# Kernel tuning notes

Hardware: AMD Instinct MI355X
Metric: run time of the kernel (lower is better)

## Reference

```python
import math
import jax, jax.numpy as jnp
import numpy as np

SHAPES = [(80, 80), (40, 40), (20, 20), (10, 10)]
BS, LQ, D, NH, NL, NP = 8, 1000, 256, 8, 4, 4
C = D // NH


def _offset_bias():
    # replicates _reset_parameters grid_init bias for sampling_offsets
    thetas = np.arange(NH, dtype=np.float32) * (2.0 * math.pi / NH)
    grid = np.stack([np.cos(thetas), np.sin(thetas)], -1)  # [NH,2]
    grid = grid / np.abs(grid).max(-1, keepdims=True)
    grid = np.tile(grid[:, None, None, :], (1, NL, NP, 1))  # [NH,NL,NP,2]
    for i in range(NP):
        grid[:, :, i, :] *= i + 1
    return jnp.asarray(grid.reshape(-1))


def setup_inputs() -> dict:
    key = jax.random.key(0)
    ks = jax.random.split(key, 8)
    len_v = sum(h * w for h, w in SHAPES)
    s = 1.0 / math.sqrt(D)
    starts = np.cumsum([0] + [h * w for h, w in SHAPES])[:-1]
    return {
        "query": jax.random.normal(ks[0], (BS, LQ, D), jnp.float32),
        "reference_points": jax.random.uniform(ks[1], (BS, LQ, NL, 2), jnp.float32),
        "value": jax.random.normal(ks[2], (BS, len_v, D), jnp.float32),
        "w_off": jax.random.normal(ks[3], (D, NH * NL * NP * 2), jnp.float32) * 0.01,
        "b_off": _offset_bias(),
        "w_attn": jax.random.normal(ks[4], (D, NH * NL * NP), jnp.float32) * 0.01,
        "b_attn": jnp.zeros((NH * NL * NP,), jnp.float32),
        "w_v": jax.random.normal(ks[5], (D, D), jnp.float32) * s,
        "b_v": jnp.zeros((D,), jnp.float32),
        "w_o": jax.random.normal(ks[6], (D, D), jnp.float32) * s,
        "b_o": jnp.zeros((D,), jnp.float32),
        "value_spatial_shapes": jnp.array(SHAPES, jnp.int32),
        "value_level_start_index": jnp.array(starts, jnp.int32),
    }


def _sample(img, grid, H, W):
    # bilinear grid_sample, padding_mode='zeros', align_corners=False
    # img: [B, C, H*W], grid: [B, Q, P, 2] in [-1, 1] -> out [B, C, Q, P]
    x = (grid[..., 0] + 1.0) * (W * 0.5) - 0.5
    y = (grid[..., 1] + 1.0) * (H * 0.5) - 0.5
    x0 = jnp.floor(x)
    y0 = jnp.floor(y)
    fx = x - x0
    fy = y - y0
    x0i = x0.astype(jnp.int32)
    y0i = y0.astype(jnp.int32)

    def gather(xi, yi, w):
        valid = (xi >= 0) & (xi < W) & (yi >= 0) & (yi < H)
        idx = jnp.clip(yi, 0, H - 1) * W + jnp.clip(xi, 0, W - 1)
        B, Q, P = idx.shape
        g = jax.vmap(lambda im, ix: im[:, ix])(img, idx.reshape(B, Q * P))  # [B,C,QP]
        return g.reshape(B, -1, Q, P) * (w * valid)[:, None]

    return (gather(x0i, y0i, (1 - fx) * (1 - fy))
            + gather(x0i + 1, y0i, fx * (1 - fy))
            + gather(x0i, y0i + 1, (1 - fx) * fy)
            + gather(x0i + 1, y0i + 1, fx * fy))


def _forward(query, reference_points, value, w_off, b_off, w_attn, b_attn,
             w_v, b_v, w_o, b_o, shapes):
    bs, lq, _ = query.shape
    v = (value @ w_v + b_v).reshape(bs, -1, NH, C)  # [bs, len_v, NH, C]
    off = (query @ w_off + b_off).reshape(bs, lq, NH, NL, NP, 2)
    attn = jax.nn.softmax((query @ w_attn + b_attn).reshape(bs, lq, NH, NL * NP), axis=-1)
    attn = attn.reshape(bs, lq, NH, NL, NP)
    # offset normalizer is spatial_shapes flipped -> (W, H) per level
    norm = jnp.array([[w, h] for h, w in shapes], dtype=query.dtype)  # [NL,2]
    loc = reference_points[:, :, None, :, None, :] + off / norm[None, None, None, :, None, :]
    grids = 2.0 * loc - 1.0  # [bs,lq,NH,NL,NP,2]
    start = 0
    sampled = []
    for lvl, (H, W) in enumerate(shapes):
        v_l = v[:, start:start + H * W].transpose(0, 2, 3, 1).reshape(bs * NH, C, H * W)
        g_l = grids[:, :, :, lvl].transpose(0, 2, 1, 3, 4).reshape(bs * NH, lq, NP, 2)
        sampled.append(_sample(v_l, g_l, H, W))  # [bs*NH, C, lq, NP]
        start += H * W
    samp = jnp.stack(sampled, axis=3).reshape(bs * NH, C, lq, NL * NP)
    aw = attn.transpose(0, 2, 1, 3, 4).reshape(bs * NH, 1, lq, NL * NP)
    out = (samp * aw).sum(-1).reshape(bs, NH * C, lq).transpose(0, 2, 1)  # [bs,lq,D]
    return out @ w_o + b_o


def reference(query, reference_points, value, w_off, b_off, w_attn, b_attn,
              w_v, b_v, w_o, b_o, value_spatial_shapes, value_level_start_index):
    shapes = [tuple(int(x) for x in r) for r in np.asarray(value_spatial_shapes)]
    return _forward(query, reference_points, value, w_off, b_off, w_attn, b_attn,
                    w_v, b_v, w_o, b_o, shapes)
```

## Files before the change

kernel.cpp:

```cpp
#include <hip/hip_runtime.h>
#include <hip/hip_bf16.h>
#include <math.h>

#define BS     8
#define LQ     1000
#define DMODEL 256
#define NH     8
#define NLV    4
#define NPT    4
#define LEN_V  8500
#define NQ     (BS*LQ)
#define MV     (BS*LEN_V)
#define KS     8

typedef __attribute__((ext_vector_type(8))) short short8;
typedef __attribute__((ext_vector_type(4))) float floatx4;

static __device__ __forceinline__ unsigned short f2bf(float f) {
    __hip_bfloat16 h = __float2bfloat16(f);
    return __builtin_bit_cast(unsigned short, h);
}
static __device__ __forceinline__ float asf(unsigned int u) {
    return __builtin_bit_cast(float, u);
}

static __device__ __forceinline__ void dma16(const unsigned short* g, unsigned short* lds) {
    __builtin_amdgcn_global_load_lds(
        (const __attribute__((address_space(1))) unsigned int*)g,
        (__attribute__((address_space(3))) unsigned int*)lds,
        16, 0, 0);
}

template <bool A32>
static __device__ __forceinline__ void gemm_core(
    const void* __restrict__ Aptr, const unsigned short* __restrict__ Bfrag,
    const float* __restrict__ bias1, const float* __restrict__ bias2, int nsplit,
    void* __restrict__ Cptr, int M, int N, int bn, int bm_start, int bm_stride,
    bool outbf, unsigned short (*As)[16384])
{
    const int tid = threadIdx.x;
    const int l   = tid & 63;
    const int w   = tid >> 6;
    const int lm  = l & 15;
    const int lk  = l >> 4;
    const int x7  = lm & 7;
    const int n_mtiles = (M + 63) >> 6;

    short8 Bf[2][KS];
    const int u0 = bn * 8 + w * 2;
    #pragma unroll
    for (int j = 0; j < 2; ++j)
        #pragma unroll
        for (int s = 0; s < KS; ++s)
            Bf[j][s] = *(const short8*)(Bfrag + ((size_t)((u0 + j) * KS + s) * 64 + l) * 8);

    auto aoff = [&](int tile, int j) -> size_t {
        const int slot = j * 256 + tid;
        const int row  = slot >> 5;
        const int gc   = (slot & 31) ^ (row & 7);
        int grow = tile * 64 + row; grow = grow < M ? grow : M - 1;
        return (size_t)grow * 256 + gc * 8;
    };

    float4 ra[8][2];

    int bm  = bm_start;
    int buf = 0;
    if (bm < n_mtiles) {
        if constexpr (A32) {
            #pragma unroll
            for (int j = 0; j < 8; ++j) {
                const float* s = (const float*)Aptr + aoff(bm, j);
                ra[j][0] = *(const float4*)s;
                ra[j][1] = *(const float4*)(s + 4);
            }
        } else {
            #pragma unroll
            for (int j = 0; j < 8; ++j)
                dma16((const unsigned short*)Aptr + aoff(bm, j),
                      &As[0][(j * 256 + w * 64) * 8]);
        }
    }

    while (bm < n_mtiles) {
        const int bm_next = bm + bm_stride;

        if constexpr (A32) {
            #pragma unroll
            for (int j = 0; j < 8; ++j) {
                const int slot = j * 256 + tid;
                short8 o;
                o[0] = (short)f2bf(ra[j][0].x); o[1] = (short)f2bf(ra[j][0].y);
                o[2] = (short)f2bf(ra[j][0].z); o[3] = (short)f2bf(ra[j][0].w);
                o[4] = (short)f2bf(ra[j][1].x); o[5] = (short)f2bf(ra[j][1].y);
                o[6] = (short)f2bf(ra[j][1].z); o[7] = (short)f2bf(ra[j][1].w);
                *(short8*)&As[buf][slot * 8] = o;
            }
            if (bm_next < n_mtiles) {
                #pragma unroll
                for (int j = 0; j < 8; ++j) {
                    const float* s = (const float*)Aptr + aoff(bm_next, j);
                    ra[j][0] = *(const float4*)s;
                    ra[j][1] = *(const float4*)(s + 4);
                }
            }
            __syncthreads();
        } else {
            __builtin_amdgcn_s_waitcnt(0);
            __syncthreads();
            if (bm_next < n_mtiles) {
                #pragma unroll
                for (int j = 0; j < 8; ++j)
                    dma16((const unsigned short*)Aptr + aoff(bm_next, j),
                          &As[buf ^ 1][(j * 256 + w * 64) * 8]);
            }
        }

        floatx4 acc[4][2];
        #pragma unroll
        for (int i = 0; i < 4; ++i)
            #pragma unroll
            for (int j = 0; j < 2; ++j)
                #pragma unroll
                for (int r = 0; r < 4; ++r) acc[i][j][r] = 0.f;

        #pragma unroll
        for (int s = 0; s < KS; ++s) {
            short8 afr[4];
            #pragma unroll
            for (int i = 0; i < 4; ++i)
                afr[i] = *(const short8*)(
                    &As[buf][(i * 16 + lm) * 256 + (((s * 4 + lk) ^ x7)) * 8]);
            #pragma unroll
            for (int i = 0; i < 4; ++i)
                #pragma unroll
                for (int j = 0; j < 2; ++j)
                    acc[i][j] = __builtin_amdgcn_mfma_f32_16x16x32_bf16(
                                    afr[i], Bf[j][s], acc[i][j], 0, 0, 0);
        }

        #pragma unroll
        for (int j = 0; j < 2; ++j) {
            const int col = bn * 128 + w * 32 + j * 16 + lm;
            const float bv = (bias2 != nullptr && col >= nsplit) ? bias2[col - nsplit]
                                                                 : bias1[col];
            #pragma unroll
            for (int i = 0; i < 4; ++i) {
                const int rbase = bm * 64 + i * 16 + lk * 4;
                #pragma unroll
                for (int r = 0; r < 4; ++r) {
                    const int row = rbase + r;
                    if (row < M) {
                        const float v = acc[i][j][r] + bv;
                        if (outbf)
                            ((unsigned short*)Cptr)[(size_t)row * N + col] = f2bf(v);
                        else
                            ((float*)Cptr)[(size_t)row * N + col] = v;
                    }
                }
            }
        }

        buf ^= 1;
        bm = bm_next;
    }
}

__global__ __launch_bounds__(256, 2) void gemm_fused(
    const float* __restrict__ value, const float* __restrict__ query,
    const unsigned short* __restrict__ wv_f, const unsigned short* __restrict__ woa_f,
    const float* __restrict__ b_v, const float* __restrict__ b_off,
    const float* __restrict__ b_attn,
    unsigned short* __restrict__ v_proj, float* __restrict__ offattn)
{
    __shared__ unsigned short As[2][16384];
    int bx = blockIdx.x;
    if (bx < 1064) {
        const int bm0 = bx % 532, bn = bx / 532;
        gemm_core<true>(value, wv_f, b_v, nullptr, 1 << 30,
                        v_proj, MV, 256, bn, bm0, 532, true, As);
    } else {
        bx -= 1064;
        const int bm0 = bx % 125, bn = bx / 125;
        gemm_core<true>(query, woa_f, b_off, b_attn, 256,
                        offattn, NQ, 384, bn, bm0, 125, false, As);
    }
}

__global__ __launch_bounds__(256, 2) void gemm_out(
    const unsigned short* __restrict__ out_pre, const unsigned short* __restrict__ wo_f,
    const float* __restrict__ b_o, float* __restrict__ out)
{
    __shared__ unsigned short As[2][16384];
    gemm_core<false>(out_pre, wo_f, b_o, nullptr, 1 << 30,
                     out, NQ, 256, blockIdx.y, blockIdx.x, 125, false, As);
}

__global__ __launch_bounds__(256) void prep_w(
    const float* __restrict__ w_v, const float* __restrict__ w_off,
    const float* __restrict__ w_attn, const float* __restrict__ w_o,
    unsigned short* __restrict__ wv_f, unsigned short* __restrict__ woa_f,
    unsigned short* __restrict__ wo_f)
{
    const int gid = blockIdx.x * 256 + threadIdx.x;
    int chunk, mode;
    if (gid < 8192)               { chunk = gid;         mode = 0; }
    else if (gid < 8192 + 12288)  { chunk = gid - 8192;  mode = 1; }
    else                          { chunk = gid - 20480; mode = 2; }
    const int l = chunk & 63, s = (chunk >> 6) & 7, u = chunk >> 9;
    short8 o;
    #pragma unroll
    for (int j = 0; j < 8; ++j) {
        const int k = s * 32 + (l >> 4) * 8 + j;
        const int n = u * 16 + (l & 15);
        float v;
        if (mode == 0)      v = w_v[k * 256 + n];
        else if (mode == 1) v = (n < 256) ? w_off[k * 256 + n] : w_attn[k * 128 + (n - 256)];
        else                v = w_o[k * 256 + n];
        o[j] = (short)f2bf(v);
    }
    unsigned short* dp = (mode == 0 ? wv_f : mode == 1 ? woa_f : wo_f)
                         + ((size_t)(u * 8 + s) * 64 + l) * 8;
    *(short8*)dp = o;
}

__global__ __launch_bounds__(512) void ms_sample_split(
    const unsigned short* __restrict__ v,
    const float* __restrict__ offattn,
    const float* __restrict__ refp,
    unsigned short* __restrict__ out_pre)
{
    __shared__ float offx_s[8][16][8];
    __shared__ float offy_s[8][16][8];
    __shared__ float atw_s [8][16][8];
    __shared__ float ref_s [8][8];
    __shared__ float part  [8][32][9];

    const int tid  = threadIdx.x;
    const int bswz = blockIdx.x & 7;
    const int iq0  = bswz * 1000 + (blockIdx.x >> 3) * 8;

    if (tid < 64) {
        const int q = tid >> 3, h = tid & 7;
        const float* rowp = offattn + (size_t)(iq0 + q) * 384;
        float lg[16];
        float m = -1e30f;
        #pragma unroll
        for (int i = 0; i < 16; ++i) { lg[i] = rowp[256 + h * 16 + i]; m = fmaxf(m, lg[i]); }
        float s = 0.f;
        #pragma unroll
        for (int i = 0; i < 16; ++i) { lg[i] = __expf(lg[i] - m); s += lg[i]; }
        const float inv = 1.f / s;
        #pragma unroll
        for (int i = 0; i < 16; ++i) atw_s[q][i][h] = lg[i] * inv;
        #pragma unroll
        for (int i = 0; i < 16; ++i) {
            offx_s[q][i][h] = rowp[(h * 16 + i) * 2 + 0];
            offy_s[q][i][h] = rowp[(h * 16 + i) * 2 + 1];
        }
        if (h == 0) {
            #pragma unroll
            for (int i = 0; i < 8; ++i) ref_s[q][i] = refp[(size_t)(iq0 + q) * 8 + i];
        }
    }
    __syncthreads();

    const int q8   = tid >> 6;
    const int half = (tid >> 5) & 1;
    const int sub  = tid & 31;
    const int h    = sub >> 2;
    const int oct  = sub & 3;

    float acc[8] = {0.f, 0.f, 0.f, 0.f, 0.f, 0.f, 0.f, 0.f};
    const unsigned short* vb = v + (size_t)bswz * LEN_V * 256 + h * 32 + oct * 8;
    const int Hs[4] = {80, 40, 20, 10};
    const int st[4] = {0, 6400, 8000, 8400};

    #pragma unroll
    for (int li = 0; li < 2; ++li) {
        const int lvl = half * 2 + li;
        const int W = Hs[lvl];
        const float bx = ref_s[q8][lvl * 2 + 0] * (float)W - 0.5f;
        const float by = ref_s[q8][lvl * 2 + 1] * (float)W - 0.5f;
        const unsigned short* vl = vb + (size_t)st[lvl] * 256;
        #pragma unroll
        for (int p = 0; p < NPT; ++p) {
            const int lp = lvl * 4 + p;
            const float x  = bx + offx_s[q8][lp][h];
            const float y  = by + offy_s[q8][lp][h];
            const float at = atw_s[q8][lp][h];
            const float x0f = floorf(x), y0f = floorf(y);
            const float fx = x - x0f, fy = y - y0f;
            const int x0 = (int)x0f, y0 = (int)y0f;
            const int x1 = x0 + 1,   y1 = y0 + 1;
            const int cx0 = min(max(x0, 0), W - 1);
            const int cx1 = min(max(x1, 0), W - 1);
            const int cy0 = min(max(y0, 0), W - 1);
            const int cy1 = min(max(y1, 0), W - 1);
            const float vx0 = (x0 >= 0 && x0 < W) ? 1.f : 0.f;
            const float vx1 = (x1 >= 0 && x1 < W) ? 1.f : 0.f;
            const float vy0 = (y0 >= 0 && y0 < W) ? 1.f : 0.f;
            const float vy1 = (y1 >= 0 && y1 < W) ? 1.f : 0.f;
            const float w00 = at * (1.f - fx) * (1.f - fy) * vx0 * vy0;
            const float w01 = at * fx * (1.f - fy) * vx1 * vy0;
            const float w10 = at * (1.f - fx) * fy * vx0 * vy1;
            const float w11 = at * fx * fy * vx1 * vy1;
            const unsigned short* r0 = vl + (size_t)(cy0 * W) * 256;
            const unsigned short* r1 = vl + (size_t)(cy1 * W) * 256;
            const uint4 d00 = *(const uint4*)(r0 + (size_t)cx0 * 256);
            const uint4 d01 = *(const uint4*)(r0 + (size_t)cx1 * 256);
            const uint4 d10 = *(const uint4*)(r1 + (size_t)cx0 * 256);
            const uint4 d11 = *(const uint4*)(r1 + (size_t)cx1 * 256);
            acc[0] += w00 * asf(d00.x << 16) + w01 * asf(d01.x << 16)
                    + w10 * asf(d10.x << 16) + w11 * asf(d11.x << 16);
            acc[1] += w00 * asf(d00.x & 0xffff0000u) + w01 * asf(d01.x & 0xffff0000u)
                    + w10 * asf(d10.x & 0xffff0000u) + w11 * asf(d11.x & 0xffff0000u);
            acc[2] += w00 * asf(d00.y << 16) + w01 * asf(d01.y << 16)
                    + w10 * asf(d10.y << 16) + w11 * asf(d11.y << 16);
            acc[3] += w00 * asf(d00.y & 0xffff0000u) + w01 * asf(d01.y & 0xffff0000u)
                    + w10 * asf(d10.y & 0xffff0000u) + w11 * asf(d11.y & 0xffff0000u);
            acc[4] += w00 * asf(d00.z << 16) + w01 * asf(d01.z << 16)
                    + w10 * asf(d10.z << 16) + w11 * asf(d11.z << 16);
            acc[5] += w00 * asf(d00.z & 0xffff0000u) + w01 * asf(d01.z & 0xffff0000u)
                    + w10 * asf(d10.z & 0xffff0000u) + w11 * asf(d11.z & 0xffff0000u);
            acc[6] += w00 * asf(d00.w << 16) + w01 * asf(d01.w << 16)
                    + w10 * asf(d10.w << 16) + w11 * asf(d11.w << 16);
            acc[7] += w00 * asf(d00.w & 0xffff0000u) + w01 * asf(d01.w & 0xffff0000u)
                    + w10 * asf(d10.w & 0xffff0000u) + w11 * asf(d11.w & 0xffff0000u);
        }
    }

    if (half == 1) {
        #pragma unroll
        for (int j = 0; j < 8; ++j) part[q8][sub][j] = acc[j];
    }
    __syncthreads();
    if (half == 0) {
        short8 o;
        #pragma unroll
        for (int j = 0; j < 8; ++j) o[j] = (short)f2bf(acc[j] + part[q8][sub][j]);
        *(short8*)(out_pre + (size_t)(iq0 + q8) * 256 + sub * 8) = o;
    }
}

extern "C" void kernel_launch(void* const* d_in, const int* in_sizes, int n_in,
                              void* d_out, int out_size, void* d_ws, size_t ws_size,
                              hipStream_t stream)
{
    const float* query  = (const float*)d_in[0];
    const float* refp   = (const float*)d_in[1];
    const float* value  = (const float*)d_in[2];
    const float* w_off  = (const float*)d_in[3];
    const float* b_off  = (const float*)d_in[4];
    const float* w_attn = (const float*)d_in[5];
    const float* b_attn = (const float*)d_in[6];
    const float* w_v    = (const float*)d_in[7];
    const float* b_v    = (const float*)d_in[8];
    const float* w_o    = (const float*)d_in[9];
    const float* b_o    = (const float*)d_in[10];
    (void)d_in[11]; (void)d_in[12];

    float* out = (float*)d_out;

    char* ws = (char*)d_ws;
    unsigned short* v_proj  = (unsigned short*)ws;
    float*          offattn = (float*)(ws + 34816000);
    unsigned short* out_pre = (unsigned short*)(ws + 47104000);
    unsigned short* wv_f    = (unsigned short*)(ws + 51200000);
    unsigned short* woa_f   = (unsigned short*)(ws + 51331072);
    unsigned short* wo_f    = (unsigned short*)(ws + 51527680);

    dim3 blk(256);

    hipLaunchKernelGGL(prep_w, dim3(112), blk, 0, stream,
                       w_v, w_off, w_attn, w_o, wv_f, woa_f, wo_f);
    hipLaunchKernelGGL(gemm_fused, dim3(1439), blk, 0, stream,
                       value, query, wv_f, woa_f, b_v, b_off, b_attn, v_proj, offattn);
    hipLaunchKernelGGL(ms_sample_split, dim3(1000), dim3(512), 0, stream,
                       v_proj, offattn, refp, out_pre);
    hipLaunchKernelGGL(gemm_out, dim3(125, 2), blk, 0, stream,
                       out_pre, wo_f, b_o, out);
}
```

Baseline: 197.1 us.

## Replace persistent double-buffered GEMM loop with one-tile-per-block GEMM kernels

```diff
diff --git a/kernel.cpp b/kernel.cpp
--- a/kernel.cpp
+++ b/kernel.cpp
@@ -32,11 +32,11 @@
 }
 
 template <bool A32>
-static __device__ __forceinline__ void gemm_core(
+static __device__ __forceinline__ void gemm_tile(
     const void* __restrict__ Aptr, const unsigned short* __restrict__ Bfrag,
     const float* __restrict__ bias1, const float* __restrict__ bias2, int nsplit,
-    void* __restrict__ Cptr, int M, int N, int bn, int bm_start, int bm_stride,
-    bool outbf, unsigned short (*As)[16384])
+    void* __restrict__ Cptr, int M, int N, int bn, int bm,
+    bool outbf, unsigned short* As )
 {
     const int tid = threadIdx.x;
     const int l   = tid & 63;
@@ -44,156 +44,125 @@
     const int lm  = l & 15;
     const int lk  = l >> 4;
     const int x7  = lm & 7;
-    const int n_mtiles = (M + 63) >> 6;
-
-    short8 Bf[2][KS];
-    const int u0 = bn * 8 + w * 2;
-    #pragma unroll
-    for (int j = 0; j < 2; ++j)
-        #pragma unroll
-        for (int s = 0; s < KS; ++s)
-            Bf[j][s] = *(const short8*)(Bfrag + ((size_t)((u0 + j) * KS + s) * 64 + l) * 8);
-
-    auto aoff = [&](int tile, int j) -> size_t {
+
+    auto aoff = [&](int j) -> size_t {
         const int slot = j * 256 + tid;
         const int row  = slot >> 5;
         const int gc   = (slot & 31) ^ (row & 7);
-        int grow = tile * 64 + row; grow = grow < M ? grow : M - 1;
+        int grow = bm * 64 + row; grow = grow < M ? grow : M - 1;
         return (size_t)grow * 256 + gc * 8;
     };
 
     float4 ra[8][2];
-
-    int bm  = bm_start;
-    int buf = 0;
-    if (bm < n_mtiles) {
-        if constexpr (A32) {
+    if constexpr (A32) {
+        #pragma unroll
+        for (int j = 0; j < 8; ++j) {
+            const float* s = (const float*)Aptr + aoff(j);
+            ra[j][0] = *(const float4*)s;
+            ra[j][1] = *(const float4*)(s + 4);
+        }
+    } else {
+        #pragma unroll
+        for (int j = 0; j < 8; ++j)
+            dma16((const unsigned short*)Aptr + aoff(j),
+                  &As[(j * 256 + w * 64) * 8]);
+    }
+
+    short8 Bf[2][KS];
+    const int u0 = bn * 8 + w * 2;
+    #pragma unroll
+    for (int j = 0; j < 2; ++j)
+        #pragma unroll
+        for (int s = 0; s < KS; ++s)
+            Bf[j][s] = *(const short8*)(Bfrag + ((size_t)((u0 + j) * KS + s) * 64 + l) * 8);
+
+    if constexpr (A32) {
+        #pragma unroll
+        for (int j = 0; j < 8; ++j) {
+            short8 o;
+            o[0] = (short)f2bf(ra[j][0].x); o[1] = (short)f2bf(ra[j][0].y);
+            o[2] = (short)f2bf(ra[j][0].z); o[3] = (short)f2bf(ra[j][0].w);
+            o[4] = (short)f2bf(ra[j][1].x); o[5] = (short)f2bf(ra[j][1].y);
+            o[6] = (short)f2bf(ra[j][1].z); o[7] = (short)f2bf(ra[j][1].w);
+            *(short8*)&As[(j * 256 + tid) * 8] = o;
+        }
+    } else {
+        __builtin_amdgcn_s_waitcnt(0);
+    }
+    __syncthreads();
+
+    floatx4 acc[4][2];
+    #pragma unroll
+    for (int i = 0; i < 4; ++i)
+        #pragma unroll
+        for (int j = 0; j < 2; ++j)
             #pragma unroll
-            for (int j = 0; j < 8; ++j) {
-                const float* s = (const float*)Aptr + aoff(bm, j);
-                ra[j][0] = *(const float4*)s;
-                ra[j][1] = *(const float4*)(s + 4);
-            }
-        } else {
-            #pragma unroll
-            for (int j = 0; j < 8; ++j)
-                dma16((const unsigned short*)Aptr + aoff(bm, j),
-                      &As[0][(j * 256 + w * 64) * 8]);
-        }
-    }
-
-    while (bm < n_mtiles) {
-        const int bm_next = bm + bm_stride;
-
-        if constexpr (A32) {
-            #pragma unroll
-            for (int j = 0; j < 8; ++j) {
-                const int slot = j * 256 + tid;
-                short8 o;
-                o[0] = (short)f2bf(ra[j][0].x); o[1] = (short)f2bf(ra[j][0].y);
-                o[2] = (short)f2bf(ra[j][0].z); o[3] = (short)f2bf(ra[j][0].w);
-                o[4] = (short)f2bf(ra[j][1].x); o[5] = (short)f2bf(ra[j][1].y);
-                o[6] = (short)f2bf(ra[j][1].z); o[7] = (short)f2bf(ra[j][1].w);
-                *(short8*)&As[buf][slot * 8] = o;
-            }
-            if (bm_next < n_mtiles) {
-                #pragma unroll
-                for (int j = 0; j < 8; ++j) {
-                    const float* s = (const float*)Aptr + aoff(bm_next, j);
-                    ra[j][0] = *(const float4*)s;
-                    ra[j][1] = *(const float4*)(s + 4);
-                }
-            }
-            __syncthreads();
-        } else {
-            __builtin_amdgcn_s_waitcnt(0);
-            __syncthreads();
-            if (bm_next < n_mtiles) {
-                #pragma unroll
-                for (int j = 0; j < 8; ++j)
-                    dma16((const unsigned short*)Aptr + aoff(bm_next, j),
-                          &As[buf ^ 1][(j * 256 + w * 64) * 8]);
-            }
-        }
-
-        floatx4 acc[4][2];
+            for (int r = 0; r < 4; ++r) acc[i][j][r] = 0.f;
+
+    #pragma unroll
+    for (int s = 0; s < KS; ++s) {
+        short8 afr[4];
+        #pragma unroll
+        for (int i = 0; i < 4; ++i)
+            afr[i] = *(const short8*)(
+                &As[(i * 16 + lm) * 256 + (((s * 4 + lk) ^ x7)) * 8]);
         #pragma unroll
         for (int i = 0; i < 4; ++i)
             #pragma unroll
             for (int j = 0; j < 2; ++j)
-                #pragma unroll
-                for (int r = 0; r < 4; ++r) acc[i][j][r] = 0.f;
-
-        #pragma unroll
-        for (int s = 0; s < KS; ++s) {
-            short8 afr[4];
+                acc[i][j] = __builtin_amdgcn_mfma_f32_16x16x32_bf16(
+                                afr[i], Bf[j][s], acc[i][j], 0, 0, 0);
+    }
+
+    #pragma unroll
+    for (int j = 0; j < 2; ++j) {
+        const int col = bn * 128 + w * 32 + j * 16 + lm;
+        const float bv = (bias2 != nullptr && col >= nsplit) ? bias2[col - nsplit]
+                                                             : bias1[col];
+        #pragma unroll
+        for (int i = 0; i < 4; ++i) {
+            const int rbase = bm * 64 + i * 16 + lk * 4;
             #pragma unroll
-            for (int i = 0; i < 4; ++i)
-                afr[i] = *(const short8*)(
-                    &As[buf][(i * 16 + lm) * 256 + (((s * 4 + lk) ^ x7)) * 8]);
-            #pragma unroll
-            for (int i = 0; i < 4; ++i)
-                #pragma unroll
-                for (int j = 0; j < 2; ++j)
-                    acc[i][j] = __builtin_amdgcn_mfma_f32_16x16x32_bf16(
-                                    afr[i], Bf[j][s], acc[i][j], 0, 0, 0);
-        }
-
-        #pragma unroll
-        for (int j = 0; j < 2; ++j) {
-            const int col = bn * 128 + w * 32 + j * 16 + lm;
-            const float bv = (bias2 != nullptr && col >= nsplit) ? bias2[col - nsplit]
-                                                                 : bias1[col];
-            #pragma unroll
-            for (int i = 0; i < 4; ++i) {
-                const int rbase = bm * 64 + i * 16 + lk * 4;
-                #pragma unroll
-                for (int r = 0; r < 4; ++r) {
-                    const int row = rbase + r;
-                    if (row < M) {
-                        const float v = acc[i][j][r] + bv;
-                        if (outbf)
-                            ((unsigned short*)Cptr)[(size_t)row * N + col] = f2bf(v);
-                        else
-                            ((float*)Cptr)[(size_t)row * N + col] = v;
-                    }
+            for (int r = 0; r < 4; ++r) {
+                const int row = rbase + r;
+                if (row < M) {
+                    const float v = acc[i][j][r] + bv;
+                    if (outbf)
+                        ((unsigned short*)Cptr)[(size_t)row * N + col] = f2bf(v);
+                    else
+                        ((float*)Cptr)[(size_t)row * N + col] = v;
                 }
             }
         }
-
-        buf ^= 1;
-        bm = bm_next;
-    }
-}
-
-__global__ __launch_bounds__(256, 2) void gemm_fused(
+    }
+}
+
+__global__ __launch_bounds__(256, 4) void gemm_fused(
     const float* __restrict__ value, const float* __restrict__ query,
     const unsigned short* __restrict__ wv_f, const unsigned short* __restrict__ woa_f,
     const float* __restrict__ b_v, const float* __restrict__ b_off,
     const float* __restrict__ b_attn,
     unsigned short* __restrict__ v_proj, float* __restrict__ offattn)
 {
-    __shared__ unsigned short As[2][16384];
+    __shared__ unsigned short As[16384];
     int bx = blockIdx.x;
-    if (bx < 1064) {
-        const int bm0 = bx % 532, bn = bx / 532;
-        gemm_core<true>(value, wv_f, b_v, nullptr, 1 << 30,
-                        v_proj, MV, 256, bn, bm0, 532, true, As);
+    if (bx < 2126) {
+        gemm_tile<true>(value, wv_f, b_v, nullptr, 1 << 30,
+                        v_proj, MV, 256, bx & 1, bx >> 1, true, As);
     } else {
-        bx -= 1064;
-        const int bm0 = bx % 125, bn = bx / 125;
-        gemm_core<true>(query, woa_f, b_off, b_attn, 256,
-                        offattn, NQ, 384, bn, bm0, 125, false, As);
-    }
-}
-
-__global__ __launch_bounds__(256, 2) void gemm_out(
+        bx -= 2126;
+        gemm_tile<true>(query, woa_f, b_off, b_attn, 256,
+                        offattn, NQ, 384, bx % 3, bx / 3, false, As);
+    }
+}
+
+__global__ __launch_bounds__(256, 4) void gemm_out(
     const unsigned short* __restrict__ out_pre, const unsigned short* __restrict__ wo_f,
     const float* __restrict__ b_o, float* __restrict__ out)
 {
-    __shared__ unsigned short As[2][16384];
-    gemm_core<false>(out_pre, wo_f, b_o, nullptr, 1 << 30,
-                     out, NQ, 256, blockIdx.y, blockIdx.x, 125, false, As);
+    __shared__ unsigned short As[16384];
+    gemm_tile<false>(out_pre, wo_f, b_o, nullptr, 1 << 30,
+                     out, NQ, 256, blockIdx.x & 1, blockIdx.x >> 1, false, As);
 }
 
 __global__ __launch_bounds__(256) void prep_w(
@@ -374,10 +343,10 @@
 
     hipLaunchKernelGGL(prep_w, dim3(112), blk, 0, stream,
                        w_v, w_off, w_attn, w_o, wv_f, woa_f, wo_f);
-    hipLaunchKernelGGL(gemm_fused, dim3(1439), blk, 0, stream,
+    hipLaunchKernelGGL(gemm_fused, dim3(2501), blk, 0, stream,
                        value, query, wv_f, woa_f, b_v, b_off, b_attn, v_proj, offattn);
     hipLaunchKernelGGL(ms_sample_split, dim3(1000), dim3(512), 0, stream,
                        v_proj, offattn, refp, out_pre);
-    hipLaunchKernelGGL(gemm_out, dim3(125, 2), blk, 0, stream,
+    hipLaunchKernelGGL(gemm_out, dim3(250), blk, 0, stream,
                        out_pre, wo_f, b_o, out);
 }
```

Measured after the change: 190.6 us. -3.3%, faster.
